# Kernel optimization log

Measured on AMD Instinct MI355X. Metric: run time of the kernel, lower is better.

Reference implementation:

```python
import jax, jax.numpy as jnp
import numpy as np

EPS = 1e-8  # torch F.cosine_similarity default eps

N, M, PLANES = 4096, 4096, 512


def setup_inputs() -> dict:
    key = jax.random.key(0)
    k1, k2, k3, k4 = jax.random.split(key, 4)
    pre = jax.random.normal(k1, (N, PLANES), dtype=jnp.float32)
    cur = jax.random.normal(k2, (M, PLANES), dtype=jnp.float32)
    adj = jax.random.uniform(k3, (N, M), dtype=jnp.float32)
    stdv = 1.0 / np.sqrt(PLANES)
    weight = jax.random.uniform(k4, (PLANES, PLANES), dtype=jnp.float32,
                                minval=-stdv, maxval=stdv)
    return {"pre": pre, "cur": cur, "adj": adj, "weight": weight}


def reference(pre, cur, adj, weight):
    # --- GraphConvolution ---
    pre_w = pre @ weight            # [N, P]
    cur_w = cur @ weight            # [M, P]
    pre_h = adj @ cur_w             # [N, P]  adj_norm @ cur_
    cur_h = adj.T @ pre_w           # [M, P]  adj_t_norm @ pre_

    # --- edge_update: tan(cosine_similarity) for all (i, j) pairs, fused ---
    # cosine_similarity(x, y) = (x . y) / (max(||x||, eps) * max(||y||, eps))
    pre_norm = jnp.maximum(jnp.linalg.norm(pre_h, axis=1, keepdims=True), EPS)
    cur_norm = jnp.maximum(jnp.linalg.norm(cur_h, axis=1, keepdims=True), EPS)
    pre_n = pre_h / pre_norm        # [N, P]
    cur_n = cur_h / cur_norm        # [M, P]
    cos = pre_n @ cur_n.T           # [N, M]
    adj_out = jnp.tan(cos)          # [N, M]
    score = adj_out.reshape(-1)     # [N*M], row-major == i * M + j ordering
    return (score, adj_out)
```

## Files before the change

### kernel.cpp

```cpp
#include <hip/hip_runtime.h>

typedef unsigned short ushort_t;
typedef __attribute__((ext_vector_type(8))) short short8;
typedef __attribute__((ext_vector_type(4))) float f32x4;

#define BK 32

__device__ __forceinline__ ushort_t f2bf(float x) {
  union { float f; unsigned u; } v; v.f = x;
  unsigned r = v.u + 0x7fffu + ((v.u >> 16) & 1u);
  return (ushort_t)(r >> 16);
}
__device__ __forceinline__ float bf2f(ushort_t h) {
  union { unsigned u; float f; } v; v.u = ((unsigned)h) << 16;
  return v.f;
}

__device__ __forceinline__ void async_cp16(const ushort_t* g, ushort_t* lds) {
  __builtin_amdgcn_global_load_lds(
      (const __attribute__((address_space(1))) unsigned int*)g,
      (__attribute__((address_space(3))) unsigned int*)lds, 16, 0, 0);
}

template <int MT, int NT, int EPI>
__device__ __forceinline__ void gemm_core(
    const ushort_t* __restrict__ A, int lda,
    const ushort_t* __restrict__ B, int ldb,
    int K,
    ushort_t* sA, ushort_t* sB,
    ushort_t* Cb, float* Cf0, float* Cf1, int ldc) {
  constexpr int MI = MT / 32, NI = NT / 32;
  const int t = threadIdx.x;
  const int wave = t >> 6, lane = t & 63;
  const int lm = lane & 15, lq = lane >> 4;
  const int wr = wave >> 1, wc = wave & 1;

  f32x4 acc[MI][NI] = {};

  const ushort_t* ga = A + (size_t)(t >> 2) * lda + (t & 3) * 8;
  const ushort_t* gb = B + (size_t)(t >> 2) * ldb + (t & 3) * 8;
  ushort_t* sA0 = sA + wave * 512;
  ushort_t* sB0 = sB + wave * 512;

  for (int k0 = 0; k0 < K; k0 += BK) {
    async_cp16(ga + k0, sA0);
    if (MT == 128) async_cp16(ga + k0 + (size_t)64 * lda, sA0 + 2048);
    async_cp16(gb + k0, sB0);
    if (NT == 128) async_cp16(gb + k0 + (size_t)64 * ldb, sB0 + 2048);
    __syncthreads();

    short8 af[MI], bf4[NI];
#pragma unroll
    for (int i = 0; i < MI; i++)
      af[i] = *(const short8*)(sA + ((wr * (MT / 2) + i * 16 + lm) * BK + lq * 8));
#pragma unroll
    for (int i = 0; i < NI; i++)
      bf4[i] = *(const short8*)(sB + ((wc * (NT / 2) + i * 16 + lm) * BK + lq * 8));
#pragma unroll
    for (int mt = 0; mt < MI; mt++)
#pragma unroll
      for (int nt = 0; nt < NI; nt++)
        acc[mt][nt] = __builtin_amdgcn_mfma_f32_16x16x32_bf16(
            af[mt], bf4[nt], acc[mt][nt], 0, 0, 0);
    __syncthreads();
  }

#pragma unroll
  for (int mt = 0; mt < MI; mt++) {
    int rb = wr * (MT / 2) + mt * 16 + lq * 4;
#pragma unroll
    for (int nt = 0; nt < NI; nt++) {
      int c = wc * (NT / 2) + nt * 16 + lm;
#pragma unroll
      for (int r = 0; r < 4; r++) {
        size_t idx = (size_t)(rb + r) * ldc + c;
        if (EPI == 1) {
          Cb[idx] = f2bf(acc[mt][nt][r]);
        } else {
          float v = __tanf(acc[mt][nt][r]);
          Cf0[idx] = v;
          Cf1[idx] = v;
        }
      }
    }
  }
}


__global__ __launch_bounds__(256) void conv_ew(
    const float* __restrict__ in, ushort_t* __restrict__ out, int n) {
  int i = (blockIdx.x * 256 + threadIdx.x) * 4;
  if (i < n) {
    float4 v = *(const float4*)(in + i);
    ushort4 o;
    o.x = f2bf(v.x); o.y = f2bf(v.y); o.z = f2bf(v.z); o.w = f2bf(v.w);
    *(ushort4*)(out + i) = o;
  }
}

__global__ __launch_bounds__(256) void convT(
    const float* __restrict__ in, ushort_t* __restrict__ outn,
    ushort_t* __restrict__ outt, int n) {
  __shared__ float tile[64][65];
  const int t = threadIdx.x;
  const int r0 = blockIdx.y * 64, c0 = blockIdx.x * 64;
  const int cr = t >> 4;
  const int cc = (t & 15) * 4;
#pragma unroll
  for (int p = 0; p < 4; p++) {
    int r = cr + p * 16;
    float4 v = *(const float4*)(in + (size_t)(r0 + r) * n + c0 + cc);
    tile[r][cc + 0] = v.x; tile[r][cc + 1] = v.y;
    tile[r][cc + 2] = v.z; tile[r][cc + 3] = v.w;
    ushort4 o;
    o.x = f2bf(v.x); o.y = f2bf(v.y); o.z = f2bf(v.z); o.w = f2bf(v.w);
    *(ushort4*)(outn + (size_t)(r0 + r) * n + c0 + cc) = o;
  }
  __syncthreads();
#pragma unroll
  for (int p = 0; p < 4; p++) {
    int r = cr + p * 16;
    ushort4 o;
    o.x = f2bf(tile[cc + 0][r]); o.y = f2bf(tile[cc + 1][r]);
    o.z = f2bf(tile[cc + 2][r]); o.w = f2bf(tile[cc + 3][r]);
    *(ushort4*)(outt + (size_t)(c0 + r) * n + r0 + cc) = o;
  }
}


__global__ __launch_bounds__(256) void k1_gemm(
    const ushort_t* __restrict__ wt_t, const ushort_t* __restrict__ pre,
    const ushort_t* __restrict__ cur, ushort_t* __restrict__ pw_t) {
  __shared__ __align__(16) ushort_t sA[64 * BK];
  __shared__ __align__(16) ushort_t sB[128 * BK];
  const int bm = blockIdx.x & 7, bn = blockIdx.x >> 3;
  const int n0 = bn * 128;
  const ushort_t* A = wt_t + (size_t)bm * 64 * 512;
  const ushort_t* B = (n0 < 4096) ? (pre + (size_t)n0 * 512)
                                  : (cur + (size_t)(n0 - 4096) * 512);
  ushort_t* C = pw_t + (size_t)bm * 64 * 8192 + n0;
  gemm_core<64, 128, 1>(A, 512, B, 512, 512, sA, sB, C, nullptr, nullptr, 8192);
}

__global__ __launch_bounds__(256) void k2_gemm(
    const ushort_t* __restrict__ adj, const ushort_t* __restrict__ adj_t,
    const ushort_t* __restrict__ pw_t, ushort_t* __restrict__ pn) {
  __shared__ __align__(16) ushort_t sA[128 * BK];
  __shared__ __align__(16) ushort_t sB[64 * BK];
  const int b = blockIdx.x;
  const int half = b >> 8, bb = b & 255;
  const int bn = (bb >> 3) & 7;
  const int bm = (bb & 7) | ((bb >> 6) << 3);
  const ushort_t* A = (half ? adj_t : adj) + (size_t)bm * 128 * 4096;
  const ushort_t* B = pw_t + (size_t)bn * 64 * 8192 + (half ? 0 : 4096);
  ushort_t* C = pn + (half ? (size_t)4096 * 512 : 0) +
                (size_t)bm * 128 * 512 + bn * 64;
  gemm_core<128, 64, 1>(A, 4096, B, 8192, 4096, sA, sB, C, nullptr, nullptr, 512);
}

__global__ __launch_bounds__(256) void rownorm_kernel(ushort_t* __restrict__ pn) {
  const int t = threadIdx.x;
  const int wave = t >> 6, lane = t & 63;
  const size_t row = (size_t)blockIdx.x * 4 + wave;
  ushort_t* p = pn + row * 512 + lane * 8;
  short8 v = *(const short8*)p;
  float f[8];
  float s = 0.f;
#pragma unroll
  for (int i = 0; i < 8; i++) {
    f[i] = bf2f((ushort_t)v[i]);
    s += f[i] * f[i];
  }
#pragma unroll
  for (int off = 32; off > 0; off >>= 1) s += __shfl_xor(s, off, 64);
  float scale = 1.0f / fmaxf(sqrtf(s), 1e-8f);
  short8 o;
#pragma unroll
  for (int i = 0; i < 8; i++) o[i] = (short)f2bf(f[i] * scale);
  *(short8*)p = o;
}

__global__ __launch_bounds__(256) void k3_gemm(
    const ushort_t* __restrict__ pn, float* __restrict__ out) {
  __shared__ __align__(16) ushort_t sA[128 * BK];
  __shared__ __align__(16) ushort_t sB[128 * BK];
  const int bm = blockIdx.x & 31, bn = blockIdx.x >> 5;
  const ushort_t* A = pn + (size_t)bm * 128 * 512;
  const ushort_t* B = pn + (size_t)4096 * 512 + (size_t)bn * 128 * 512;
  float* C0 = out + (size_t)bm * 128 * 4096 + bn * 128;
  gemm_core<128, 128, 2>(A, 512, B, 512, 512, sA, sB, nullptr, C0,
                         C0 + (size_t)4096 * 4096, 4096);
}

extern "C" void kernel_launch(void* const* d_in, const int* in_sizes, int n_in,
                              void* d_out, int out_size, void* d_ws,
                              size_t ws_size, hipStream_t stream) {
  const float* pre = (const float*)d_in[0];
  const float* cur = (const float*)d_in[1];
  const float* adj = (const float*)d_in[2];
  const float* wt  = (const float*)d_in[3];
  float* out = (float*)d_out;

  ushort_t* adj_bf = (ushort_t*)d_ws;
  ushort_t* adj_t  = adj_bf + (size_t)4096 * 4096;
  ushort_t* pw_t   = adj_t + (size_t)4096 * 4096;
  ushort_t* pn     = pw_t + (size_t)512 * 8192;
  ushort_t* wt_t   = pn + (size_t)8192 * 512;
  ushort_t* wt_bf  = wt_t + (size_t)512 * 512;
  ushort_t* pre_bf = wt_bf + (size_t)512 * 512;
  ushort_t* cur_bf = pre_bf + (size_t)4096 * 512;

  conv_ew<<<2048, 256, 0, stream>>>(pre, pre_bf, 4096 * 512);
  conv_ew<<<2048, 256, 0, stream>>>(cur, cur_bf, 4096 * 512);
  convT<<<dim3(64, 64), 256, 0, stream>>>(adj, adj_bf, adj_t, 4096);
  convT<<<dim3(8, 8), 256, 0, stream>>>(wt, wt_bf, wt_t, 512);
  k1_gemm<<<512, 256, 0, stream>>>(wt_t, pre_bf, cur_bf, pw_t);
  k2_gemm<<<512, 256, 0, stream>>>(adj_bf, adj_t, pw_t, pn);
  rownorm_kernel<<<2048, 256, 0, stream>>>(pn);
  k3_gemm<<<1024, 256, 0, stream>>>(pn, out);
}
```

Baseline: 336.6 us.

## Fuse input bf16 conversion into k1, defer row normalization to k3 epilogue, widen k2 K-tile

Removes the two elementwise pre/cur conversion kernels: k1 now loads fp32 pre/cur directly, converts to bf16 in registers and writes the result to LDS. The rownorm kernel no longer rewrites pn. It only produces per-row inverse norms, which the k3 epilogue applies before tan. The GEMM core gains a configurable K-tile, and k2 uses BK=64 to halve the barrier count per K step. Risks: k1 now does synchronous global loads in place of async copies, and the result differs slightly in rounding because normalization is no longer applied before the bf16 rounding of pn.

```diff
diff --git a/kernel.cpp b/kernel.cpp
--- a/kernel.cpp
+++ b/kernel.cpp
@@ -3,8 +3,6 @@
 typedef unsigned short ushort_t;
 typedef __attribute__((ext_vector_type(8))) short short8;
 typedef __attribute__((ext_vector_type(4))) float f32x4;
-
-#define BK 32
 
 __device__ __forceinline__ ushort_t f2bf(float x) {
   union { float f; unsigned u; } v; v.f = x;
@@ -22,14 +20,17 @@
       (__attribute__((address_space(3))) unsigned int*)lds, 16, 0, 0);
 }
 
-template <int MT, int NT, int EPI>
+template <int MT, int NT, int BKT, int EPI>
 __device__ __forceinline__ void gemm_core(
     const ushort_t* __restrict__ A, int lda,
     const ushort_t* __restrict__ B, int ldb,
     int K,
     ushort_t* sA, ushort_t* sB,
-    ushort_t* Cb, float* Cf0, float* Cf1, int ldc) {
-  constexpr int MI = MT / 32, NI = NT / 32;
+    ushort_t* Cb, float* Cf0, float* Cf1, int ldc,
+    const float* __restrict__ ip, const float* __restrict__ ic) {
+  constexpr int MI = MT / 32, NI = NT / 32, KU = BKT / 32;
+  constexpr int LPR = BKT / 8;
+  constexpr int RPC = 256 / LPR;
   const int t = threadIdx.x;
   const int wave = t >> 6, lane = t & 63;
   const int lm = lane & 15, lq = lane >> 4;
@@ -37,31 +38,38 @@
 
   f32x4 acc[MI][NI] = {};
 
-  const ushort_t* ga = A + (size_t)(t >> 2) * lda + (t & 3) * 8;
-  const ushort_t* gb = B + (size_t)(t >> 2) * ldb + (t & 3) * 8;
+  const ushort_t* ga = A + (size_t)(t / LPR) * lda + (t % LPR) * 8;
+  const ushort_t* gb = B + (size_t)(t / LPR) * ldb + (t % LPR) * 8;
   ushort_t* sA0 = sA + wave * 512;
   ushort_t* sB0 = sB + wave * 512;
 
-  for (int k0 = 0; k0 < K; k0 += BK) {
-    async_cp16(ga + k0, sA0);
-    if (MT == 128) async_cp16(ga + k0 + (size_t)64 * lda, sA0 + 2048);
-    async_cp16(gb + k0, sB0);
-    if (NT == 128) async_cp16(gb + k0 + (size_t)64 * ldb, sB0 + 2048);
-    __syncthreads();
-
-    short8 af[MI], bf4[NI];
-#pragma unroll
-    for (int i = 0; i < MI; i++)
-      af[i] = *(const short8*)(sA + ((wr * (MT / 2) + i * 16 + lm) * BK + lq * 8));
-#pragma unroll
-    for (int i = 0; i < NI; i++)
-      bf4[i] = *(const short8*)(sB + ((wc * (NT / 2) + i * 16 + lm) * BK + lq * 8));
-#pragma unroll
-    for (int mt = 0; mt < MI; mt++)
-#pragma unroll
-      for (int nt = 0; nt < NI; nt++)
-        acc[mt][nt] = __builtin_amdgcn_mfma_f32_16x16x32_bf16(
-            af[mt], bf4[nt], acc[mt][nt], 0, 0, 0);
+  for (int k0 = 0; k0 < K; k0 += BKT) {
+#pragma unroll
+    for (int j = 0; j < MT / RPC; j++)
+      async_cp16(ga + k0 + (size_t)j * RPC * lda, sA0 + j * 2048);
+#pragma unroll
+    for (int j = 0; j < NT / RPC; j++)
+      async_cp16(gb + k0 + (size_t)j * RPC * ldb, sB0 + j * 2048);
+    __syncthreads();
+
+#pragma unroll
+    for (int ku = 0; ku < KU; ku++) {
+      short8 af[MI], bf4[NI];
+#pragma unroll
+      for (int i = 0; i < MI; i++)
+        af[i] = *(const short8*)(sA + (wr * (MT / 2) + i * 16 + lm) * BKT +
+                                 ku * 32 + lq * 8);
+#pragma unroll
+      for (int i = 0; i < NI; i++)
+        bf4[i] = *(const short8*)(sB + (wc * (NT / 2) + i * 16 + lm) * BKT +
+                                  ku * 32 + lq * 8);
+#pragma unroll
+      for (int mt = 0; mt < MI; mt++)
+#pragma unroll
+        for (int nt = 0; nt < NI; nt++)
+          acc[mt][nt] = __builtin_amdgcn_mfma_f32_16x16x32_bf16(
+              af[mt], bf4[nt], acc[mt][nt], 0, 0, 0);
+    }
     __syncthreads();
   }
 
@@ -77,24 +85,12 @@
         if (EPI == 1) {
           Cb[idx] = f2bf(acc[mt][nt][r]);
         } else {
-          float v = __tanf(acc[mt][nt][r]);
+          float v = __tanf(acc[mt][nt][r] * ip[rb + r] * ic[c]);
           Cf0[idx] = v;
           Cf1[idx] = v;
         }
       }
     }
-  }
-}
-
-
-__global__ __launch_bounds__(256) void conv_ew(
-    const float* __restrict__ in, ushort_t* __restrict__ out, int n) {
-  int i = (blockIdx.x * 256 + threadIdx.x) * 4;
-  if (i < n) {
-    float4 v = *(const float4*)(in + i);
-    ushort4 o;
-    o.x = f2bf(v.x); o.y = f2bf(v.y); o.z = f2bf(v.z); o.w = f2bf(v.w);
-    *(ushort4*)(out + i) = o;
   }
 }
 
@@ -127,26 +123,81 @@
   }
 }
 
-
 __global__ __launch_bounds__(256) void k1_gemm(
-    const ushort_t* __restrict__ wt_t, const ushort_t* __restrict__ pre,
-    const ushort_t* __restrict__ cur, ushort_t* __restrict__ pw_t) {
-  __shared__ __align__(16) ushort_t sA[64 * BK];
-  __shared__ __align__(16) ushort_t sB[128 * BK];
+    const ushort_t* __restrict__ wt_t, const float* __restrict__ pre,
+    const float* __restrict__ cur, ushort_t* __restrict__ pw_t) {
+  __shared__ __align__(16) ushort_t sA[64 * 32];
+  __shared__ __align__(16) ushort_t sB[128 * 32];
+  const int t = threadIdx.x;
+  const int wave = t >> 6, lane = t & 63;
+  const int lm = lane & 15, lq = lane >> 4;
+  const int wr = wave >> 1, wc = wave & 1;
   const int bm = blockIdx.x & 7, bn = blockIdx.x >> 3;
   const int n0 = bn * 128;
   const ushort_t* A = wt_t + (size_t)bm * 64 * 512;
-  const ushort_t* B = (n0 < 4096) ? (pre + (size_t)n0 * 512)
-                                  : (cur + (size_t)(n0 - 4096) * 512);
+  const float* Bf = (n0 < 4096) ? (pre + (size_t)n0 * 512)
+                                : (cur + (size_t)(n0 - 4096) * 512);
   ushort_t* C = pw_t + (size_t)bm * 64 * 8192 + n0;
-  gemm_core<64, 128, 1>(A, 512, B, 512, 512, sA, sB, C, nullptr, nullptr, 8192);
+
+  f32x4 acc[2][4] = {};
+  const ushort_t* ga = A + (size_t)(t >> 2) * 512 + (t & 3) * 8;
+  const float* gb = Bf + (size_t)(t >> 2) * 512 + (t & 3) * 8;
+  ushort_t* sA0 = sA + wave * 512;
+  ushort_t* sBw = sB + t * 8;
+
+  for (int k0 = 0; k0 < 512; k0 += 32) {
+    async_cp16(ga + k0, sA0);
+    float4 u0 = *(const float4*)(gb + k0);
+    float4 u1 = *(const float4*)(gb + k0 + 4);
+    float4 u2 = *(const float4*)(gb + k0 + (size_t)64 * 512);
+    float4 u3 = *(const float4*)(gb + k0 + (size_t)64 * 512 + 4);
+    short8 w0, w1;
+    w0[0] = (short)f2bf(u0.x); w0[1] = (short)f2bf(u0.y);
+    w0[2] = (short)f2bf(u0.z); w0[3] = (short)f2bf(u0.w);
+    w0[4] = (short)f2bf(u1.x); w0[5] = (short)f2bf(u1.y);
+    w0[6] = (short)f2bf(u1.z); w0[7] = (short)f2bf(u1.w);
+    w1[0] = (short)f2bf(u2.x); w1[1] = (short)f2bf(u2.y);
+    w1[2] = (short)f2bf(u2.z); w1[3] = (short)f2bf(u2.w);
+    w1[4] = (short)f2bf(u3.x); w1[5] = (short)f2bf(u3.y);
+    w1[6] = (short)f2bf(u3.z); w1[7] = (short)f2bf(u3.w);
+    *(short8*)(sBw) = w0;
+    *(short8*)(sBw + 2048) = w1;
+    __syncthreads();
+
+    short8 af[2], bf4[4];
+#pragma unroll
+    for (int i = 0; i < 2; i++)
+      af[i] = *(const short8*)(sA + (wr * 32 + i * 16 + lm) * 32 + lq * 8);
+#pragma unroll
+    for (int i = 0; i < 4; i++)
+      bf4[i] = *(const short8*)(sB + (wc * 64 + i * 16 + lm) * 32 + lq * 8);
+#pragma unroll
+    for (int mt = 0; mt < 2; mt++)
+#pragma unroll
+      for (int nt = 0; nt < 4; nt++)
+        acc[mt][nt] = __builtin_amdgcn_mfma_f32_16x16x32_bf16(
+            af[mt], bf4[nt], acc[mt][nt], 0, 0, 0);
+    __syncthreads();
+  }
+
+#pragma unroll
+  for (int mt = 0; mt < 2; mt++) {
+    int rb = wr * 32 + mt * 16 + lq * 4;
+#pragma unroll
+    for (int nt = 0; nt < 4; nt++) {
+      int c = wc * 64 + nt * 16 + lm;
+#pragma unroll
+      for (int r = 0; r < 4; r++)
+        C[(size_t)(rb + r) * 8192 + c] = f2bf(acc[mt][nt][r]);
+    }
+  }
 }
 
 __global__ __launch_bounds__(256) void k2_gemm(
     const ushort_t* __restrict__ adj, const ushort_t* __restrict__ adj_t,
     const ushort_t* __restrict__ pw_t, ushort_t* __restrict__ pn) {
-  __shared__ __align__(16) ushort_t sA[128 * BK];
-  __shared__ __align__(16) ushort_t sB[64 * BK];
+  __shared__ __align__(16) ushort_t sA[128 * 64];
+  __shared__ __align__(16) ushort_t sB[64 * 64];
   const int b = blockIdx.x;
   const int half = b >> 8, bb = b & 255;
   const int bn = (bb >> 3) & 7;
@@ -155,41 +206,40 @@
   const ushort_t* B = pw_t + (size_t)bn * 64 * 8192 + (half ? 0 : 4096);
   ushort_t* C = pn + (half ? (size_t)4096 * 512 : 0) +
                 (size_t)bm * 128 * 512 + bn * 64;
-  gemm_core<128, 64, 1>(A, 4096, B, 8192, 4096, sA, sB, C, nullptr, nullptr, 512);
-}
-
-__global__ __launch_bounds__(256) void rownorm_kernel(ushort_t* __restrict__ pn) {
+  gemm_core<128, 64, 64, 1>(A, 4096, B, 8192, 4096, sA, sB, C, nullptr,
+                            nullptr, 512, nullptr, nullptr);
+}
+
+__global__ __launch_bounds__(256) void invnorm_kernel(
+    const ushort_t* __restrict__ pn, float* __restrict__ invn) {
   const int t = threadIdx.x;
   const int wave = t >> 6, lane = t & 63;
   const size_t row = (size_t)blockIdx.x * 4 + wave;
-  ushort_t* p = pn + row * 512 + lane * 8;
+  const ushort_t* p = pn + row * 512 + lane * 8;
   short8 v = *(const short8*)p;
-  float f[8];
   float s = 0.f;
 #pragma unroll
   for (int i = 0; i < 8; i++) {
-    f[i] = bf2f((ushort_t)v[i]);
-    s += f[i] * f[i];
+    float f = bf2f((ushort_t)v[i]);
+    s += f * f;
   }
 #pragma unroll
   for (int off = 32; off > 0; off >>= 1) s += __shfl_xor(s, off, 64);
-  float scale = 1.0f / fmaxf(sqrtf(s), 1e-8f);
-  short8 o;
-#pragma unroll
-  for (int i = 0; i < 8; i++) o[i] = (short)f2bf(f[i] * scale);
-  *(short8*)p = o;
+  if (lane == 0) invn[row] = 1.0f / fmaxf(sqrtf(s), 1e-8f);
 }
 
 __global__ __launch_bounds__(256) void k3_gemm(
-    const ushort_t* __restrict__ pn, float* __restrict__ out) {
-  __shared__ __align__(16) ushort_t sA[128 * BK];
-  __shared__ __align__(16) ushort_t sB[128 * BK];
+    const ushort_t* __restrict__ pn, const float* __restrict__ invn,
+    float* __restrict__ out) {
+  __shared__ __align__(16) ushort_t sA[128 * 32];
+  __shared__ __align__(16) ushort_t sB[128 * 32];
   const int bm = blockIdx.x & 31, bn = blockIdx.x >> 5;
   const ushort_t* A = pn + (size_t)bm * 128 * 512;
   const ushort_t* B = pn + (size_t)4096 * 512 + (size_t)bn * 128 * 512;
   float* C0 = out + (size_t)bm * 128 * 4096 + bn * 128;
-  gemm_core<128, 128, 2>(A, 512, B, 512, 512, sA, sB, nullptr, C0,
-                         C0 + (size_t)4096 * 4096, 4096);
+  gemm_core<128, 128, 32, 2>(A, 512, B, 512, 512, sA, sB, nullptr, C0,
+                             C0 + (size_t)4096 * 4096, 4096,
+                             invn + bm * 128, invn + 4096 + bn * 128);
 }
 
 extern "C" void kernel_launch(void* const* d_in, const int* in_sizes, int n_in,
@@ -207,15 +257,12 @@
   ushort_t* pn     = pw_t + (size_t)512 * 8192;
   ushort_t* wt_t   = pn + (size_t)8192 * 512;
   ushort_t* wt_bf  = wt_t + (size_t)512 * 512;
-  ushort_t* pre_bf = wt_bf + (size_t)512 * 512;
-  ushort_t* cur_bf = pre_bf + (size_t)4096 * 512;
-
-  conv_ew<<<2048, 256, 0, stream>>>(pre, pre_bf, 4096 * 512);
-  conv_ew<<<2048, 256, 0, stream>>>(cur, cur_bf, 4096 * 512);
+  float*    invn   = (float*)(wt_bf + (size_t)512 * 512);
+
   convT<<<dim3(64, 64), 256, 0, stream>>>(adj, adj_bf, adj_t, 4096);
   convT<<<dim3(8, 8), 256, 0, stream>>>(wt, wt_bf, wt_t, 512);
-  k1_gemm<<<512, 256, 0, stream>>>(wt_t, pre_bf, cur_bf, pw_t);
+  k1_gemm<<<512, 256, 0, stream>>>(wt_t, pre, cur, pw_t);
   k2_gemm<<<512, 256, 0, stream>>>(adj_bf, adj_t, pw_t, pn);
-  rownorm_kernel<<<2048, 256, 0, stream>>>(pn);
-  k3_gemm<<<1024, 256, 0, stream>>>(pn, out);
-}
+  invnorm_kernel<<<2048, 256, 0, stream>>>(pn, invn);
+  k3_gemm<<<1024, 256, 0, stream>>>(pn, invn, out);
+}
```

After: 333.6 us. Within noise of the previous version (-0.9%).
